# Kernel optimization log

Measured on AMD Instinct MI355X. Metric: run time of the kernel, lower is better.

The kernel has to match this reference:

```python
import jax, jax.numpy as jnp
import numpy as np

N_NODES = 50000
N_EDGES = 800000
D_FEAT = 96
OUT_DIM = 96


def setup_inputs() -> dict:
    key = jax.random.key(0)
    k1, k2, k3, k4 = jax.random.split(key, 4)
    x = jax.random.normal(k1, (N_NODES, D_FEAT), dtype=jnp.float32)
    W = jax.random.normal(k2, (D_FEAT, OUT_DIM), dtype=jnp.float32) / np.sqrt(D_FEAT)
    b = jnp.zeros((OUT_DIM,), dtype=jnp.float32)
    src = jax.random.randint(k3, (N_EDGES,), 0, N_NODES, dtype=jnp.int64)
    dst = jax.random.randint(k4, (N_EDGES,), 0, N_NODES, dtype=jnp.int64)
    return {"x": x, "W": W, "b": b, "src": src, "dst": dst}


def reference(x, W, b, src, dst):
    # GCNConv: symmetric degree normalization, transform-then-aggregate.
    ones = jnp.ones(src.shape[0], dtype=x.dtype)
    deg_out = jax.ops.segment_sum(ones, src, num_segments=N_NODES)  # [N]
    deg_in = jax.ops.segment_sum(ones, dst, num_segments=N_NODES)   # [N]
    inv_sqrt_out = jnp.where(deg_out > 0, jax.lax.rsqrt(deg_out), 0.0)
    inv_sqrt_in = jnp.where(deg_in > 0, jax.lax.rsqrt(deg_in), 0.0)

    h = x @ W  # [N, out_dim] - transform first (cheap GEMM)
    coef = inv_sqrt_out[src] * inv_sqrt_in[dst]         # [E]
    msg = h[src] * coef[:, None]                         # [E, out_dim] gather
    agg = jax.ops.segment_sum(msg, dst, num_segments=N_NODES)  # scatter-reduce
    return agg + b
```

## Files before the change

kernel.cpp:

```cpp
#include <hip/hip_runtime.h>

#define N_NODES 50000
#define N_EDGES 800000
#define DFEAT 96

#define RBITS  14
#define RSIZE  16384
#define HWORDS (RSIZE / 2)
#define NRANGE 4
#define NCHUNK 64
#define CHUNK_E (N_EDGES / NCHUNK)
#define HF_BLOCKS (NRANGE * NCHUNK)
#define NB 196

typedef short bf16x8 __attribute__((ext_vector_type(8)));
typedef float f32x4  __attribute__((ext_vector_type(4)));

__device__ __forceinline__ unsigned bpack(float a, float b) {
    unsigned ua = __float_as_uint(a);
    unsigned ub = __float_as_uint(b);
    ua = (ua + 0x7FFFu + ((ua >> 16) & 1u)) >> 16;
    ub = (ub + 0x7FFFu + ((ub >> 16) & 1u)) >> 16;
    return ua | (ub << 16);
}
__device__ __forceinline__ unsigned short b1(float a) {
    unsigned u = __float_as_uint(a);
    u = (u + 0x7FFFu + ((u >> 16) & 1u)) >> 16;
    return (unsigned short)u;
}

__global__ __launch_bounds__(512) void deg_hist_kernel(
    const int* __restrict__ src, const int* __restrict__ dst,
    unsigned* __restrict__ ptab) {
    __shared__ unsigned hh[HWORDS];
    int tid = threadIdx.x;
    int r = blockIdx.x & (NRANGE - 1);
    int c = blockIdx.x >> 2;
    for (int i = tid; i < HWORDS; i += 512) hh[i] = 0;
    __syncthreads();
    int lo = r << RBITS;
    const int4* s4 = (const int4*)(src + c * CHUNK_E);
    const int4* d4 = (const int4*)(dst + c * CHUNK_E);
    for (int i = tid; i < CHUNK_E / 4; i += 512) {
        int4 s = s4[i];
        int4 d = d4[i];
        unsigned a;
        a = (unsigned)(s.x - lo); if (a < RSIZE) atomicAdd(&hh[a >> 1], 1u << ((a & 1) << 4));
        a = (unsigned)(s.y - lo); if (a < RSIZE) atomicAdd(&hh[a >> 1], 1u << ((a & 1) << 4));
        a = (unsigned)(s.z - lo); if (a < RSIZE) atomicAdd(&hh[a >> 1], 1u << ((a & 1) << 4));
        a = (unsigned)(s.w - lo); if (a < RSIZE) atomicAdd(&hh[a >> 1], 1u << ((a & 1) << 4));
        a = (unsigned)(d.x - lo); if (a < RSIZE) atomicAdd(&hh[a >> 1], 0x100u << ((a & 1) << 4));
        a = (unsigned)(d.y - lo); if (a < RSIZE) atomicAdd(&hh[a >> 1], 0x100u << ((a & 1) << 4));
        a = (unsigned)(d.z - lo); if (a < RSIZE) atomicAdd(&hh[a >> 1], 0x100u << ((a & 1) << 4));
        a = (unsigned)(d.w - lo); if (a < RSIZE) atomicAdd(&hh[a >> 1], 0x100u << ((a & 1) << 4));
    }
    __syncthreads();
    unsigned* pt = ptab + ((size_t)blockIdx.x << (RBITS - 1));
    for (int i = tid; i < HWORDS; i += 512) pt[i] = hh[i];
}

__global__ __launch_bounds__(256) void deg_reduce_kernel(
    const unsigned* __restrict__ ptab, unsigned short* __restrict__ pfx,
    int* __restrict__ deg_out, int* __restrict__ deg_in,
    int* __restrict__ bsum) {
    __shared__ int ws[4];
    int tid = threadIdx.x;
    int n = blockIdx.x * 256 + tid;
    int so = 0, si = 0;
    if (n < N_NODES) {
        int r = n >> RBITS, bin = n & (RSIZE - 1);
        int w = bin >> 1, sh = (bin & 1) << 4;
        #pragma unroll 8
        for (int c = 0; c < NCHUNK; ++c) {
            unsigned v = (ptab[(((size_t)(c * NRANGE + r)) << (RBITS - 1)) + w] >> sh) & 0xffffu;
            so += (int)(v & 0xffu);
            pfx[(((size_t)(c * NRANGE + r)) << RBITS) + bin] = (unsigned short)si;
            si += (int)(v >> 8);
        }
        deg_out[n] = so;
        deg_in[n]  = si;
    }
    int v = si;
    #pragma unroll
    for (int off = 32; off; off >>= 1) v += __shfl_down(v, off, 64);
    if ((tid & 63) == 0) ws[tid >> 6] = v;
    __syncthreads();
    if (tid == 0) bsum[blockIdx.x] = ws[0] + ws[1] + ws[2] + ws[3];
}

__global__ __launch_bounds__(256) void scan_final_kernel(
    const int* __restrict__ deg, const int* __restrict__ bsum,
    int* __restrict__ offs, int nb) {
    __shared__ int wsum[4];
    __shared__ int sbase;
    int tid = threadIdx.x, lane = tid & 63, wave = tid >> 6;
    int i = blockIdx.x * 256 + tid;
    int v = (i < N_NODES) ? deg[i] : 0;
    int x = v;
    #pragma unroll
    for (int off = 1; off < 64; off <<= 1) {
        int t = __shfl_up(x, off, 64);
        if (lane >= off) x += t;
    }
    if (lane == 63) wsum[wave] = x;
    if (wave == 0) {
        int s = 0;
        for (int j = lane; j < blockIdx.x; j += 64) s += bsum[j];
        #pragma unroll
        for (int off = 32; off; off >>= 1) s += __shfl_down(s, off, 64);
        if (lane == 0) sbase = s;
    }
    if (blockIdx.x == gridDim.x - 1 && wave == 1) {
        int s = 0;
        for (int j = lane; j < nb; j += 64) s += bsum[j];
        #pragma unroll
        for (int off = 32; off; off >>= 1) s += __shfl_down(s, off, 64);
        if (lane == 0) offs[N_NODES] = s;
    }
    __syncthreads();
    int wb = sbase;
    for (int w = 0; w < wave; ++w) wb += wsum[w];
    if (i < N_NODES) offs[i] = wb + x - v;
}

#define GROWS 128
#define NGB ((N_NODES + GROWS - 1) / GROWS)
#define TLD 104

union FGSm {
    unsigned cur[HWORDS];
    struct {
        unsigned short WT[96 * TLD];
        unsigned short xA[GROWS * TLD];
    } g;
};

__global__ __launch_bounds__(512) void fill_gemm_kernel(
    const int* __restrict__ src, const int* __restrict__ dst,
    const int* __restrict__ offs, const unsigned short* __restrict__ pfx,
    int* __restrict__ csr_src,
    const float* __restrict__ x, const float* __restrict__ W,
    const int* __restrict__ deg_out, unsigned short* __restrict__ h, int nrows) {
    __shared__ FGSm sm;
    int tid = threadIdx.x;

    if (blockIdx.x < HF_BLOCKS) {
        int r = blockIdx.x & (NRANGE - 1);
        int c = blockIdx.x >> 2;
        int lo = r << RBITS;
        const unsigned short* pf = pfx + ((size_t)blockIdx.x << RBITS);
        for (int i = tid; i < HWORDS; i += 512)
            sm.cur[i] = *(const unsigned*)&pf[2 * i];
        __syncthreads();
        const int4* s4 = (const int4*)(src + c * CHUNK_E);
        const int4* d4 = (const int4*)(dst + c * CHUNK_E);
        for (int i = tid; i < CHUNK_E / 4; i += 512) {
            int4 s = s4[i];
            int4 d = d4[i];
            unsigned a, old, rank;
            a = (unsigned)(d.x - lo);
            if (a < RSIZE) {
                old = atomicAdd(&sm.cur[a >> 1], 1u << ((a & 1) << 4));
                rank = (old >> ((a & 1) << 4)) & 0xffffu;
                csr_src[offs[lo + a] + rank] = s.x;
            }
            a = (unsigned)(d.y - lo);
            if (a < RSIZE) {
                old = atomicAdd(&sm.cur[a >> 1], 1u << ((a & 1) << 4));
                rank = (old >> ((a & 1) << 4)) & 0xffffu;
                csr_src[offs[lo + a] + rank] = s.y;
            }
            a = (unsigned)(d.z - lo);
            if (a < RSIZE) {
                old = atomicAdd(&sm.cur[a >> 1], 1u << ((a & 1) << 4));
                rank = (old >> ((a & 1) << 4)) & 0xffffu;
                csr_src[offs[lo + a] + rank] = s.z;
            }
            a = (unsigned)(d.w - lo);
            if (a < RSIZE) {
                old = atomicAdd(&sm.cur[a >> 1], 1u << ((a & 1) << 4));
                rank = (old >> ((a & 1) << 4)) & 0xffffu;
                csr_src[offs[lo + a] + rank] = s.w;
            }
        }
        return;
    }

    int r0 = (blockIdx.x - HF_BLOCKS) * GROWS;

    for (int i = tid; i < 48 * 96; i += 512) {
        int k2 = i / 96, n = i - k2 * 96;
        float w0 = W[(size_t)(2 * k2) * 96 + n];
        float w1 = W[(size_t)(2 * k2 + 1) * 96 + n];
        *(unsigned*)&sm.g.WT[n * TLD + 2 * k2] = bpack(w0, w1);
    }
    for (int i = tid; i < GROWS * 24; i += 512) {
        int m = i / 24, k4 = i - m * 24;
        int row = r0 + m; if (row >= nrows) row = nrows - 1;
        float4 v = *(const float4*)&x[(size_t)row * 96 + 4 * k4];
        *(unsigned*)&sm.g.xA[m * TLD + 4 * k4]     = bpack(v.x, v.y);
        *(unsigned*)&sm.g.xA[m * TLD + 4 * k4 + 2] = bpack(v.z, v.w);
    }
    __syncthreads();

    int lane = tid & 63, wave = tid >> 6;
    int m16 = lane & 15;
    int g = lane >> 4;
    int rbase = wave * 16;

    bf16x8 afrag[3];
    #pragma unroll
    for (int ks = 0; ks < 3; ++ks)
        afrag[ks] = *(const bf16x8*)&sm.g.xA[(rbase + m16) * TLD + ks * 32 + g * 8];

    f32x4 acc[6];
    #pragma unroll
    for (int nt = 0; nt < 6; ++nt) {
        f32x4 c = {0.f, 0.f, 0.f, 0.f};
        #pragma unroll
        for (int ks = 0; ks < 3; ++ks) {
            bf16x8 bfrag = *(const bf16x8*)&sm.g.WT[(nt * 16 + m16) * TLD + ks * 32 + g * 8];
            c = __builtin_amdgcn_mfma_f32_16x16x32_bf16(afrag[ks], bfrag, c, 0, 0, 0);
        }
        acc[nt] = c;
    }

    float sc[4];
    #pragma unroll
    for (int r = 0; r < 4; ++r) {
        int row = r0 + rbase + g * 4 + r;
        int d = (row < nrows) ? deg_out[row] : 1;
        sc[r] = (d > 0) ? rsqrtf((float)d) : 0.f;
    }
    #pragma unroll
    for (int nt = 0; nt < 6; ++nt) {
        #pragma unroll
        for (int r = 0; r < 4; ++r) {
            int row = r0 + rbase + g * 4 + r;
            if (row < nrows)
                h[(size_t)row * 96 + nt * 16 + m16] = b1(acc[nt][r] * sc[r]);
        }
    }
}

__device__ __forceinline__ void upadd(float* a, uint4 q) {
    a[0] += __uint_as_float(q.x << 16);
    a[1] += __uint_as_float(q.x & 0xffff0000u);
    a[2] += __uint_as_float(q.y << 16);
    a[3] += __uint_as_float(q.y & 0xffff0000u);
    a[4] += __uint_as_float(q.z << 16);
    a[5] += __uint_as_float(q.z & 0xffff0000u);
    a[6] += __uint_as_float(q.w << 16);
    a[7] += __uint_as_float(q.w & 0xffff0000u);
}

#define AGG_NODES 16
#define IDX_CAP 2048
__global__ __launch_bounds__(256) void agg_kernel(
    const unsigned short* __restrict__ h, const int* __restrict__ csr_src,
    const int* __restrict__ offs, const float* __restrict__ b,
    float* __restrict__ out) {
    __shared__ int sh_idx[IDX_CAP];
    __shared__ int sh_off[AGG_NODES + 1];
    int tid = threadIdx.x;
    int n0 = blockIdx.x * AGG_NODES;
    if (tid <= AGG_NODES) sh_off[tid] = offs[n0 + tid];
    __syncthreads();
    int s0 = sh_off[0];
    int len = sh_off[AGG_NODES] - s0;
    bool lds_ok = (len <= IDX_CAP);
    if (lds_ok) {
        for (int i = tid; i < len; i += 256) sh_idx[i] = csr_src[s0 + i];
    }
    __syncthreads();

    int node = tid >> 4;
    int lane16 = tid & 15;
    int j = lane16 & 3;
    int q = lane16 >> 2;
    int start = sh_off[node], end = sh_off[node + 1];
    float acc[24];
    #pragma unroll
    for (int i = 0; i < 24; ++i) acc[i] = 0.f;
    const uint4* hb = (const uint4*)h;

    int e = start + q;
    for (; e + 4 < end; e += 8) {
        int i0 = lds_ok ? sh_idx[e - s0] : csr_src[e];
        int i1 = lds_ok ? sh_idx[e + 4 - s0] : csr_src[e + 4];
        size_t b0 = (size_t)i0 * 12 + j;
        size_t b1 = (size_t)i1 * 12 + j;
        uint4 q0 = hb[b0], q1 = hb[b0 + 4], q2 = hb[b0 + 8];
        uint4 p0 = hb[b1], p1 = hb[b1 + 4], p2 = hb[b1 + 8];
        upadd(acc + 0, q0); upadd(acc + 8, q1); upadd(acc + 16, q2);
        upadd(acc + 0, p0); upadd(acc + 8, p1); upadd(acc + 16, p2);
    }
    if (e < end) {
        int i0 = lds_ok ? sh_idx[e - s0] : csr_src[e];
        size_t b0 = (size_t)i0 * 12 + j;
        uint4 q0 = hb[b0], q1 = hb[b0 + 4], q2 = hb[b0 + 8];
        upadd(acc + 0, q0); upadd(acc + 8, q1); upadd(acc + 16, q2);
    }
    #pragma unroll
    for (int i = 0; i < 24; ++i) {
        acc[i] += __shfl_xor(acc[i], 4, 64);
        acc[i] += __shfl_xor(acc[i], 8, 64);
    }
    if (q != 0) return;
    float inv = (end > start) ? rsqrtf((float)(end - start)) : 0.f;
    int n = n0 + node;
    #pragma unroll
    for (int g = 0; g < 3; ++g) {
        int slot = j + 4 * g;
        float4 bb0 = *(const float4*)(b + 8 * slot);
        float4 bb1 = *(const float4*)(b + 8 * slot + 4);
        float4 r0, r1;
        r0.x = acc[g * 8 + 0] * inv + bb0.x;
        r0.y = acc[g * 8 + 1] * inv + bb0.y;
        r0.z = acc[g * 8 + 2] * inv + bb0.z;
        r0.w = acc[g * 8 + 3] * inv + bb0.w;
        r1.x = acc[g * 8 + 4] * inv + bb1.x;
        r1.y = acc[g * 8 + 5] * inv + bb1.y;
        r1.z = acc[g * 8 + 6] * inv + bb1.z;
        r1.w = acc[g * 8 + 7] * inv + bb1.w;
        float4* o = (float4*)(out + (size_t)n * DFEAT + 8 * slot);
        o[0] = r0; o[1] = r1;
    }
}

extern "C" void kernel_launch(void* const* d_in, const int* in_sizes, int n_in,
                              void* d_out, int out_size, void* d_ws, size_t ws_size,
                              hipStream_t stream) {
    const float* x  = (const float*)d_in[0];
    const float* W  = (const float*)d_in[1];
    const float* b  = (const float*)d_in[2];
    const int*   src = (const int*)d_in[3];
    const int*   dst = (const int*)d_in[4];
    float* out = (float*)d_out;

    int* deg_out = (int*)d_ws;
    int* deg_in  = deg_out + N_NODES;
    int* offs    = deg_in + N_NODES;
    int* csr_src = offs + N_NODES + 1;
    int* bsum    = csr_src + N_EDGES;
    size_t off1 = (((size_t)(3 * N_NODES + 1 + N_EDGES + 256)) * 4 + 255) & ~(size_t)255;
    unsigned* ptab = (unsigned*)((char*)d_ws + off1);
    size_t off2 = off1 + ((size_t)HF_BLOCKS << (RBITS - 1)) * 4;
    unsigned short* pfx = (unsigned short*)((char*)d_ws + off2);
    size_t off3 = (off2 + ((size_t)HF_BLOCKS << RBITS) * 2 + 255) & ~(size_t)255;
    unsigned short* h = (unsigned short*)((char*)d_ws + off3);

    deg_hist_kernel<<<HF_BLOCKS, 512, 0, stream>>>(src, dst, ptab);
    deg_reduce_kernel<<<NB, 256, 0, stream>>>(ptab, pfx, deg_out, deg_in, bsum);
    scan_final_kernel<<<NB, 256, 0, stream>>>(deg_in, bsum, offs, NB);
    fill_gemm_kernel<<<HF_BLOCKS + NGB, 512, 0, stream>>>(
        src, dst, offs, pfx, csr_src, x, W, deg_out, h, N_NODES);
    agg_kernel<<<N_NODES / AGG_NODES, 256, 0, stream>>>(h, csr_src, offs, b, out);
}
```

Measured before the change: 134.5 us.

## Fuse degree reduce and scan via decoupled lookback; halve histogram ranges

The degree-reduce and scan kernels become one kernel. Each block publishes its block sum through a flag array with release semantics, and later blocks spin on earlier flags to get their prefix base, which removes one kernel launch and the deg_in round trip. Separately, the histogram range grows to 32768 nodes, so there are 2 ranges instead of 4. That halves the histogram and fill block count but doubles shared-memory histogram size per block, which may reduce occupancy and parallelism. The spin-wait relies on all 196 blocks being co-resident or scheduled in order.

```diff
diff --git a/kernel.cpp b/kernel.cpp
--- a/kernel.cpp
+++ b/kernel.cpp
@@ -4,10 +4,10 @@
 #define N_EDGES 800000
 #define DFEAT 96
 
-#define RBITS  14
-#define RSIZE  16384
+#define RBITS  15
+#define RSIZE  32768
 #define HWORDS (RSIZE / 2)
-#define NRANGE 4
+#define NRANGE 2
 #define NCHUNK 64
 #define CHUNK_E (N_EDGES / NCHUNK)
 #define HF_BLOCKS (NRANGE * NCHUNK)
@@ -31,11 +31,16 @@
 
 __global__ __launch_bounds__(512) void deg_hist_kernel(
     const int* __restrict__ src, const int* __restrict__ dst,
-    unsigned* __restrict__ ptab) {
+    unsigned* __restrict__ ptab, unsigned long long* __restrict__ bflag) {
     __shared__ unsigned hh[HWORDS];
     int tid = threadIdx.x;
     int r = blockIdx.x & (NRANGE - 1);
-    int c = blockIdx.x >> 2;
+    int c = blockIdx.x >> 1;
+    if (tid == 0) {
+        if ((int)blockIdx.x < NB) bflag[blockIdx.x] = 0ULL;
+        int k = blockIdx.x + HF_BLOCKS;
+        if (k < NB) bflag[k] = 0ULL;
+    }
     for (int i = tid; i < HWORDS; i += 512) hh[i] = 0;
     __syncthreads();
     int lo = r << RBITS;
@@ -59,12 +64,13 @@
     for (int i = tid; i < HWORDS; i += 512) pt[i] = hh[i];
 }
 
-__global__ __launch_bounds__(256) void deg_reduce_kernel(
+__global__ __launch_bounds__(256) void deg_scan_kernel(
     const unsigned* __restrict__ ptab, unsigned short* __restrict__ pfx,
-    int* __restrict__ deg_out, int* __restrict__ deg_in,
-    int* __restrict__ bsum) {
-    __shared__ int ws[4];
-    int tid = threadIdx.x;
+    int* __restrict__ deg_out, int* __restrict__ offs,
+    unsigned long long* __restrict__ bflag) {
+    __shared__ int wsc[4];
+    __shared__ int sbase;
+    int tid = threadIdx.x, lane = tid & 63, wave = tid >> 6;
     int n = blockIdx.x * 256 + tid;
     int so = 0, si = 0;
     if (n < N_NODES) {
@@ -78,49 +84,38 @@
             si += (int)(v >> 8);
         }
         deg_out[n] = so;
-        deg_in[n]  = si;
-    }
-    int v = si;
-    #pragma unroll
-    for (int off = 32; off; off >>= 1) v += __shfl_down(v, off, 64);
-    if ((tid & 63) == 0) ws[tid >> 6] = v;
-    __syncthreads();
-    if (tid == 0) bsum[blockIdx.x] = ws[0] + ws[1] + ws[2] + ws[3];
-}
-
-__global__ __launch_bounds__(256) void scan_final_kernel(
-    const int* __restrict__ deg, const int* __restrict__ bsum,
-    int* __restrict__ offs, int nb) {
-    __shared__ int wsum[4];
-    __shared__ int sbase;
-    int tid = threadIdx.x, lane = tid & 63, wave = tid >> 6;
-    int i = blockIdx.x * 256 + tid;
-    int v = (i < N_NODES) ? deg[i] : 0;
-    int x = v;
+    }
+    int x = si;
     #pragma unroll
     for (int off = 1; off < 64; off <<= 1) {
         int t = __shfl_up(x, off, 64);
         if (lane >= off) x += t;
     }
-    if (lane == 63) wsum[wave] = x;
+    if (lane == 63) wsc[wave] = x;
+    __syncthreads();
+    int bs = wsc[0] + wsc[1] + wsc[2] + wsc[3];
+    if (tid == 0)
+        __hip_atomic_store(&bflag[blockIdx.x],
+                           (((unsigned long long)(unsigned)bs) << 1) | 1ULL,
+                           __ATOMIC_RELEASE, __HIP_MEMORY_SCOPE_AGENT);
     if (wave == 0) {
         int s = 0;
-        for (int j = lane; j < blockIdx.x; j += 64) s += bsum[j];
+        for (int j2 = lane; j2 < (int)blockIdx.x; j2 += 64) {
+            unsigned long long v;
+            do {
+                v = __hip_atomic_load(&bflag[j2], __ATOMIC_ACQUIRE, __HIP_MEMORY_SCOPE_AGENT);
+            } while (!(v & 1ULL));
+            s += (int)(v >> 1);
+        }
         #pragma unroll
         for (int off = 32; off; off >>= 1) s += __shfl_down(s, off, 64);
         if (lane == 0) sbase = s;
     }
-    if (blockIdx.x == gridDim.x - 1 && wave == 1) {
-        int s = 0;
-        for (int j = lane; j < nb; j += 64) s += bsum[j];
-        #pragma unroll
-        for (int off = 32; off; off >>= 1) s += __shfl_down(s, off, 64);
-        if (lane == 0) offs[N_NODES] = s;
-    }
     __syncthreads();
     int wb = sbase;
-    for (int w = 0; w < wave; ++w) wb += wsum[w];
-    if (i < N_NODES) offs[i] = wb + x - v;
+    for (int w2 = 0; w2 < wave; ++w2) wb += wsc[w2];
+    if (n < N_NODES) offs[n] = wb + x - si;
+    if (blockIdx.x == NB - 1 && tid == 0) offs[N_NODES] = sbase + bs;
 }
 
 #define GROWS 128
@@ -146,7 +141,7 @@
 
     if (blockIdx.x < HF_BLOCKS) {
         int r = blockIdx.x & (NRANGE - 1);
-        int c = blockIdx.x >> 2;
+        int c = blockIdx.x >> 1;
         int lo = r << RBITS;
         const unsigned short* pf = pfx + ((size_t)blockIdx.x << RBITS);
         for (int i = tid; i < HWORDS; i += 512)
@@ -339,20 +334,19 @@
     float* out = (float*)d_out;
 
     int* deg_out = (int*)d_ws;
-    int* deg_in  = deg_out + N_NODES;
-    int* offs    = deg_in + N_NODES;
+    int* offs    = deg_out + N_NODES;
     int* csr_src = offs + N_NODES + 1;
-    int* bsum    = csr_src + N_EDGES;
-    size_t off1 = (((size_t)(3 * N_NODES + 1 + N_EDGES + 256)) * 4 + 255) & ~(size_t)255;
+    size_t off0 = (((size_t)(2 * N_NODES + 1 + N_EDGES)) * 4 + 255) & ~(size_t)255;
+    unsigned long long* bflag = (unsigned long long*)((char*)d_ws + off0);
+    size_t off1 = (off0 + NB * 8 + 255) & ~(size_t)255;
     unsigned* ptab = (unsigned*)((char*)d_ws + off1);
     size_t off2 = off1 + ((size_t)HF_BLOCKS << (RBITS - 1)) * 4;
     unsigned short* pfx = (unsigned short*)((char*)d_ws + off2);
     size_t off3 = (off2 + ((size_t)HF_BLOCKS << RBITS) * 2 + 255) & ~(size_t)255;
     unsigned short* h = (unsigned short*)((char*)d_ws + off3);
 
-    deg_hist_kernel<<<HF_BLOCKS, 512, 0, stream>>>(src, dst, ptab);
-    deg_reduce_kernel<<<NB, 256, 0, stream>>>(ptab, pfx, deg_out, deg_in, bsum);
-    scan_final_kernel<<<NB, 256, 0, stream>>>(deg_in, bsum, offs, NB);
+    deg_hist_kernel<<<HF_BLOCKS, 512, 0, stream>>>(src, dst, ptab, bflag);
+    deg_scan_kernel<<<NB, 256, 0, stream>>>(ptab, pfx, deg_out, offs, bflag);
     fill_gemm_kernel<<<HF_BLOCKS + NGB, 512, 0, stream>>>(
         src, dst, offs, pfx, csr_src, x, W, deg_out, h, N_NODES);
     agg_kernel<<<N_NODES / AGG_NODES, 256, 0, stream>>>(h, csr_src, offs, b, out);
```

New measurement: 142.8 us. 1.06x slower.
